# Optimization experiments

Measured on AMD Instinct MI355X. Metric: run time of the kernel, lower is better.

## Reference

```python
import jax, jax.numpy as jnp
import numpy as np

B, T, NR = 64, 128, 2
L, H, D = 8, 8, 512
HD = D // H
TMAX = T + 1  # block_size: U buffer has t+1 entries
U0 = jnp.array([191.713, 215.888], dtype=jnp.float32)


def _ln(x, w, b):
    mu = x.mean(-1, keepdims=True)
    var = ((x - mu) ** 2).mean(-1, keepdims=True)
    return (x - mu) * jax.lax.rsqrt(var + 1e-5) * w + b


def setup_inputs() -> dict:
    key = jax.random.key(0)
    ks = jax.random.split(key, 24)
    s = 0.02
    inp = {
        'data': jax.random.uniform(ks[0], (B, 4), jnp.float32),
        'r': jax.random.normal(ks[1], (B, T, NR), jnp.float32),
        'y_d': jax.random.normal(ks[2], (B, T, NR), jnp.float32),
        # token encoder: concat(e, u) -> D
        'wte_w': s * jax.random.normal(ks[3], (2 * NR, D), jnp.float32),
        'wte_b': jnp.zeros((D,), jnp.float32),
        'wpe': s * jax.random.normal(ks[4], (TMAX, D), jnp.float32),
        'ln1_w': jnp.ones((L, D), jnp.float32),
        'ln1_b': jnp.zeros((L, D), jnp.float32),
        'qkv_w': s * jax.random.normal(ks[5], (L, D, 3 * D), jnp.float32),
        'qkv_b': jnp.zeros((L, 3 * D), jnp.float32),
        'proj_w': s * jax.random.normal(ks[6], (L, D, D), jnp.float32),
        'proj_b': jnp.zeros((L, D), jnp.float32),
        'ln2_w': jnp.ones((L, D), jnp.float32),
        'ln2_b': jnp.zeros((L, D), jnp.float32),
        'fc_w': s * jax.random.normal(ks[7], (L, D, 4 * D), jnp.float32),
        'fc_b': jnp.zeros((L, 4 * D), jnp.float32),
        'mproj_w': s * jax.random.normal(ks[8], (L, 4 * D, D), jnp.float32),
        'mproj_b': jnp.zeros((L, D), jnp.float32),
        'lnf_w': jnp.ones((D,), jnp.float32),
        'lnf_b': jnp.zeros((D,), jnp.float32),
        'head_w': s * jax.random.normal(ks[9], (D, NR), jnp.float32),
        'head_b': jnp.zeros((NR,), jnp.float32),
    }
    return inp


def reference(data, r, y_d, wte_w, wte_b, wpe, ln1_w, ln1_b, qkv_w, qkv_b,
              proj_w, proj_b, ln2_w, ln2_b, fc_w, fc_b, mproj_w, mproj_b,
              lnf_w, lnf_b, head_w, head_b):
    # Incremental GPT decode with KV cache; math identical to recomputing
    # causal attention over the growing [E, U] prefix at every step.
    def gpt_step(token, pos, K, V):
        h = token @ wte_w + wte_b + wpe[pos]  # [B, D]
        for l in range(L):
            hn = _ln(h, ln1_w[l], ln1_b[l])
            qkv = hn @ qkv_w[l] + qkv_b[l]
            q, k, v = jnp.split(qkv, 3, axis=-1)
            q = q.reshape(B, H, HD)
            K = K.at[l, :, :, pos].set(k.reshape(B, H, HD))
            V = V.at[l, :, :, pos].set(v.reshape(B, H, HD))
            sc = jnp.einsum('bhd,bhtd->bht', q, K[l]) / jnp.sqrt(jnp.float32(HD))
            valid = jnp.arange(TMAX) <= pos
            sc = jnp.where(valid[None, None, :], sc, -jnp.inf)
            att = jax.nn.softmax(sc, axis=-1)
            o = jnp.einsum('bht,bhtd->bhd', att, V[l]).reshape(B, D)
            h = h + o @ proj_w[l] + proj_b[l]
            hn2 = _ln(h, ln2_w[l], ln2_b[l])
            h = h + jax.nn.gelu(hn2 @ fc_w[l] + fc_b[l], approximate=False) @ mproj_w[l] + mproj_b[l]
        h = _ln(h, lnf_w, lnf_b)
        return h @ head_w + head_b, K, V

    a_par = data[:, :NR]        # tmp params -> dynamics: x_dot = -a*x + b*u
    b_par = data[:, NR:2 * NR]

    def step(carry, r_i):
        y, u, K, V, i = carry
        e = r_i - y                       # e_i = r_i - y_i
        tok = jnp.concatenate([e, u], axis=-1)
        u_next, K, V = gpt_step(tok, i, K, V)
        x_dot = -a_par * y + b_par * u_next  # Ts = 1 Euler step
        y_next = y + x_dot
        return (y_next, u_next, K, V, i + 1), y

    K0 = jnp.zeros((L, B, H, TMAX, HD), jnp.float32)
    V0 = jnp.zeros((L, B, H, TMAX, HD), jnp.float32)
    u0 = jnp.broadcast_to(U0, (B, NR))
    y0 = y_d[:, 0, :]
    _, Y = jax.lax.scan(step, (y0, u0, K0, V0, jnp.int32(0)), jnp.swapaxes(r, 0, 1))
    return jnp.swapaxes(Y, 0, 1)  # [B, T, NR]
```

## Files before the change

kernel.cpp:

```cpp
#include <hip/hip_runtime.h>
#include <hip/hip_bf16.h>
#include <math.h>
#include <stdio.h>

#define NWG 256
#define NT  512
#define T_  128
#define L_  8
typedef unsigned short ushort_t;

struct P {
  const float *data,*r,*y_d,*wte_w,*wte_b,*wpe,*ln1_w,*ln1_b,*qkv_w,*qkv_b,
              *proj_w,*proj_b,*ln2_w,*ln2_b,*fc_w,*fc_b,*mproj_w,*mproj_b,
              *lnf_w,*lnf_b,*head_w,*head_b;
  float *out, *y, *u, *h0, *h1;
  ushort_t *qT, *oT, *gT;
  ushort_t *wq, *wp, *wf, *wm;
  ushort_t *Kc, *Vc;
  unsigned long long *sync;
};

__device__ __forceinline__ float bf2f(ushort_t u) {
  return __uint_as_float(((unsigned)u) << 16);
}
__device__ __forceinline__ ushort_t f2bf(float f) {
  __hip_bfloat16 b = __float2bfloat16(f);
  return *reinterpret_cast<ushort_t*>(&b);
}

__global__ void wconv(const float* __restrict__ src, ushort_t* __restrict__ dst, int n) {
  int i = blockIdx.x * blockDim.x + threadIdx.x;
  const int stride = gridDim.x * blockDim.x;
  for (; i < n; i += stride) dst[i] = f2bf(src[i]);
}

__device__ __forceinline__ void gbar(unsigned long long* gs, int xcd) {
  __syncthreads();
  if (threadIdx.x == 0) {
    unsigned long long* leaf = gs + xcd * 16;
    unsigned long long* root = gs + 128;
    unsigned long long* gen  = gs + 144;
    const unsigned long long g0 = __hip_atomic_load(gen, __ATOMIC_RELAXED, __HIP_MEMORY_SCOPE_AGENT);
    const unsigned long long lo = __hip_atomic_fetch_add(leaf, 1ULL, __ATOMIC_RELAXED, __HIP_MEMORY_SCOPE_AGENT);
    if (lo == 31ULL) {
      __hip_atomic_store(leaf, 0ULL, __ATOMIC_RELAXED, __HIP_MEMORY_SCOPE_AGENT);
      const unsigned long long ro = __hip_atomic_fetch_add(root, 1ULL, __ATOMIC_RELEASE, __HIP_MEMORY_SCOPE_AGENT);
      if (ro == 7ULL) {
        __hip_atomic_store(root, 0ULL, __ATOMIC_RELAXED, __HIP_MEMORY_SCOPE_AGENT);
        __hip_atomic_fetch_add(gen, 1ULL, __ATOMIC_RELEASE, __HIP_MEMORY_SCOPE_AGENT);
      }
    }
    while (__hip_atomic_load(gen, __ATOMIC_RELAXED, __HIP_MEMORY_SCOPE_AGENT) == g0)
      __builtin_amdgcn_s_sleep(2);
    (void)__hip_atomic_load(gen, __ATOMIC_ACQUIRE, __HIP_MEMORY_SCOPE_AGENT);
  }
  __syncthreads();
}

__device__ __forceinline__ int swz4(int k) { return ((k >> 1) & 3); }

__device__ __forceinline__ void stage_bf(const ushort_t* __restrict__ src, int W,
                                         int row0, int k0, float* slab) {
  const int tid = threadIdx.x;
  const int m = tid >> 5, q = tid & 31;
  const ushort_t* sp = src + (size_t)(row0 + m) * W + k0;
  #pragma unroll
  for (int i = 0; i < 16; ++i) {
    const int k = q + i * 32;
    slab[k * 16 + (m ^ (swz4(k) << 2))] = bf2f(sp[k]);
  }
}

__device__ __forceinline__ void stats_ln(const float* __restrict__ h,
                                         const float* __restrict__ lnw,
                                         const float* __restrict__ lnb,
                                         int rb, float* slab) {
  const int tid = threadIdx.x;
  const int m = tid >> 5, q = tid & 31;
  const float* hp = h + (size_t)(rb * 16 + m) * 512;
  float vv[16];
  float s = 0.f, s2 = 0.f;
  #pragma unroll
  for (int i = 0; i < 16; ++i) {
    const int k = q + i * 32;
    const float v = hp[k];
    vv[i] = v; s += v; s2 += v * v;
  }
  #pragma unroll
  for (int mk = 1; mk <= 16; mk <<= 1) { s += __shfl_xor(s, mk); s2 += __shfl_xor(s2, mk); }
  const float mu = s * (1.f / 512.f);
  const float rs = rsqrtf(s2 * (1.f / 512.f) - mu * mu + 1e-5f);
  #pragma unroll
  for (int i = 0; i < 16; ++i) {
    const int k = q + i * 32;
    slab[k * 16 + (m ^ (swz4(k) << 2))] = (vv[i] - mu) * rs * lnw[k] + lnb[k];
  }
}

#define FMA_ALL(W_, A_) \
  A_[0]+=W_*a0.x; A_[1]+=W_*a0.y; A_[2]+=W_*a0.z; A_[3]+=W_*a0.w; \
  A_[4]+=W_*a1.x; A_[5]+=W_*a1.y; A_[6]+=W_*a1.z; A_[7]+=W_*a1.w; \
  A_[8]+=W_*a2.x; A_[9]+=W_*a2.y; A_[10]+=W_*a2.z; A_[11]+=W_*a2.w; \
  A_[12]+=W_*a3.x; A_[13]+=W_*a3.y; A_[14]+=W_*a3.z; A_[15]+=W_*a3.w;

template<int N>
__device__ __forceinline__ void gemm_acc(const ushort_t* __restrict__ Wbase,
                                         const float* __restrict__ slab,
                                         float* acc0, float* acc1) {
  const int tid = threadIdx.x;
  const int wv = tid >> 6, lane = tid & 63;
  const int kq = lane >> 4, cp = lane & 15;
  const int r0 = wv * 64 + kq;
  const ushort_t* Wg = Wbase + (size_t)r0 * N + cp * 2;
  unsigned w[16];
  #pragma unroll
  for (int u = 0; u < 16; ++u)
    w[u] = *(const unsigned*)(Wg + (size_t)(u * 4) * N);
  #pragma unroll
  for (int u = 0; u < 16; ++u) {
    const int row = r0 + u * 4;
    const float4* b4 = (const float4*)(slab + row * 16);
    const int c4 = swz4(row);
    const float4 a0 = b4[0 ^ c4], a1 = b4[1 ^ c4], a2 = b4[2 ^ c4], a3 = b4[3 ^ c4];
    const float wx = bf2f((ushort_t)w[u]), wy = bf2f((ushort_t)(w[u] >> 16));
    FMA_ALL(wx, acc0)
    FMA_ALL(wy, acc1)
  }
}

__device__ __forceinline__ float gemm_finish(float* acc0, float* acc1, float* redw) {
  const int tid = threadIdx.x;
  const int wv = tid >> 6, lane = tid & 63;
  #pragma unroll
  for (int m = 0; m < 16; ++m) {
    acc0[m] += __shfl_xor(acc0[m], 16); acc1[m] += __shfl_xor(acc1[m], 16);
    acc0[m] += __shfl_xor(acc0[m], 32); acc1[m] += __shfl_xor(acc1[m], 32);
  }
  if (lane < 16) {
    float* rp = redw + wv * 528 + lane * 33;
    #pragma unroll
    for (int m = 0; m < 16; ++m) { rp[m] = acc0[m]; rp[16 + m] = acc1[m]; }
  }
  __syncthreads();
  const int col = tid & 31, m2 = tid >> 5;
  float s = 0.f;
  #pragma unroll
  for (int w2 = 0; w2 < 8; ++w2)
    s += redw[w2 * 528 + (col >> 1) * 33 + (col & 1) * 16 + m2];
  return s;
}

#define ACC_INIT float acc0[16], acc1[16]; \
  _Pragma("unroll") for (int m_ = 0; m_ < 16; ++m_) { acc0[m_] = 0.f; acc1[m_] = 0.f; }

__global__ __launch_bounds__(NT, 1) void gptloop(P p) {
  const int bid = blockIdx.x, tid = threadIdx.x;
  const int xcd = bid & 7, slot = bid >> 3;
  unsigned long long* sb = p.sync;

  __shared__ float slab[8192];
  __shared__ float redw[8 * 528];
  __shared__ float red1[512], red2[512];
  __shared__ float att_s[2][128];
  __shared__ float qv_s[2][64];
  __shared__ float inv_s[2];
  __shared__ float bc[4];

  if (slot < 8) {
    const int b = xcd * 8 + slot, t = tid;
    const float y0 = p.y_d[b * 256], y1 = p.y_d[b * 256 + 1];
    const float e0 = p.r[b * 256] - y0, e1 = p.r[b * 256 + 1] - y1;
    p.h0[b * 512 + t] = e0 * p.wte_w[t] + e1 * p.wte_w[512 + t]
                      + 191.713f * p.wte_w[1024 + t] + 215.888f * p.wte_w[1536 + t]
                      + p.wte_b[t] + p.wpe[t];
    if (t < 2) {
      p.y[b * 2 + t] = t ? y1 : y0;
      p.u[b * 2 + t] = t ? 215.888f : 191.713f;
    }
  }
  gbar(sb, xcd);

  for (int st = 0; st < T_; ++st) {
    for (int l = 0; l < L_; ++l) {
      if (slot < 24) {
        const int cb = xcd * 6 + (slot >> 2), rb = slot & 3;
        stats_ln(p.h0, p.ln1_w + l * 512, p.ln1_b + l * 512, rb, slab);
        __syncthreads();
        ACC_INIT
        gemm_acc<1536>(p.wq + (size_t)l * 786432 + cb * 32, slab, acc0, acc1);
        float v = gemm_finish(acc0, acc1, redw);
        const int col = tid & 31, m = tid >> 5;
        const int gcol = cb * 32 + col;
        v += p.qkv_b[l * 1536 + gcol];
        const int part = gcol >> 9, head = (gcol & 511) >> 6, off = gcol & 63;
        const int b = rb * 16 + m;
        if (part == 0) {
          p.qT[b * 512 + gcol] = f2bf(v * 0.125f);
        } else {
          ushort_t* dst = (part == 1) ? p.Kc : p.Vc;
          dst[((size_t)(l * 64 + b) * 8 + head) * 8192 + st * 64 + off] = f2bf(v);
        }
      }
      gbar(sb, xcd);

      {
        const int pp = tid >> 8, t = tid & 255;
        const int pid = bid * 2 + pp, b = pid >> 3, hh = pid & 7;
        const size_t kvb = ((size_t)(l * 64 + b) * 8 + hh) * (size_t)8192;
        if (t < 64) qv_s[pp][t] = bf2f(p.qT[b * 512 + hh * 64 + t]);
        __syncthreads();
        float s = -1e30f;
        if (t <= st && t < 128) {
          const uint4* kp = (const uint4*)(p.Kc + kvb + (size_t)t * 64);
          float sc = 0.f;
          #pragma unroll
          for (int j2 = 0; j2 < 8; ++j2) {
            const uint4 k4 = kp[j2];
            sc += qv_s[pp][j2*8+0] * bf2f((ushort_t)k4.x)
                + qv_s[pp][j2*8+1] * bf2f((ushort_t)(k4.x >> 16))
                + qv_s[pp][j2*8+2] * bf2f((ushort_t)k4.y)
                + qv_s[pp][j2*8+3] * bf2f((ushort_t)(k4.y >> 16))
                + qv_s[pp][j2*8+4] * bf2f((ushort_t)k4.z)
                + qv_s[pp][j2*8+5] * bf2f((ushort_t)(k4.z >> 16))
                + qv_s[pp][j2*8+6] * bf2f((ushort_t)k4.w)
                + qv_s[pp][j2*8+7] * bf2f((ushort_t)(k4.w >> 16));
          }
          s = sc;
        }
        red1[tid] = s; __syncthreads();
        for (int s2 = 128; s2 >= 1; s2 >>= 1) {
          if (t < s2) red1[tid] = fmaxf(red1[tid], red1[tid + s2]);
          __syncthreads();
        }
        const float mx = red1[pp * 256];
        __syncthreads();
        const float e = (t <= st && t < 128) ? expf(s - mx) : 0.f;
        if (t < 128) att_s[pp][t] = e;
        red1[tid] = e; __syncthreads();
        for (int s2 = 128; s2 >= 1; s2 >>= 1) {
          if (t < s2) red1[tid] += red1[tid + s2];
          __syncthreads();
        }
        if (t == 0) inv_s[pp] = 1.f / red1[pp * 256];
        __syncthreads();
        const int d = t & 63, tq = t >> 6;
        float o = 0.f;
        for (int tt = tq; tt <= st; tt += 4)
          o += att_s[pp][tt] * bf2f(p.Vc[kvb + (size_t)tt * 64 + d]);
        red1[tid] = o; __syncthreads();
        if (tid < 128) {
          const int p2 = tid >> 6, d2 = tid & 63;
          const int pid2 = bid * 2 + p2, b2 = pid2 >> 3, h2 = pid2 & 7;
          const float oo = (red1[p2*256 + d2] + red1[p2*256 + 64 + d2]
                          + red1[p2*256 + 128 + d2] + red1[p2*256 + 192 + d2]) * inv_s[p2];
          p.oT[b2 * 512 + h2 * 64 + d2] = f2bf(oo);
        }
      }
      gbar(sb, xcd);

      if (slot < 8) {
        const int cb = xcd * 2 + (slot >> 2), rb = slot & 3;
        stage_bf(p.oT, 512, rb * 16, 0, slab);
        __syncthreads();
        ACC_INIT
        gemm_acc<512>(p.wp + (size_t)l * 262144 + cb * 32, slab, acc0, acc1);
        const float v = gemm_finish(acc0, acc1, redw);
        const int col = tid & 31, m = tid >> 5;
        const int gcol = cb * 32 + col, row = rb * 16 + m;
        p.h1[row * 512 + gcol] = p.h0[row * 512 + gcol] + v + p.proj_b[l * 512 + gcol];
      }
      gbar(sb, xcd);

      {
        const int cb = xcd * 8 + (slot >> 2), rb = slot & 3;
        stats_ln(p.h1, p.ln2_w + l * 512, p.ln2_b + l * 512, rb, slab);
        __syncthreads();
        ACC_INIT
        gemm_acc<2048>(p.wf + (size_t)l * 1048576 + cb * 32, slab, acc0, acc1);
        const float v = gemm_finish(acc0, acc1, redw);
        const int col = tid & 31, m = tid >> 5;
        const int gcol = cb * 32 + col;
        const float x = v + p.fc_b[l * 2048 + gcol];
        p.gT[(size_t)(rb * 16 + m) * 2048 + gcol] =
            f2bf(0.5f * x * (1.f + erff(x * 0.70710678118654752f)));
      }
      gbar(sb, xcd);

      if (slot < 8) {
        const int cb = xcd * 2 + (slot >> 2), rb = slot & 3;
        ACC_INIT
        for (int ch = 0; ch < 4; ++ch) {
          __syncthreads();
          stage_bf(p.gT, 2048, rb * 16, ch * 512, slab);
          __syncthreads();
          gemm_acc<512>(p.wm + (size_t)l * 1048576 + (size_t)(ch * 512) * 512 + cb * 32,
                        slab, acc0, acc1);
        }
        const float v = gemm_finish(acc0, acc1, redw);
        const int col = tid & 31, m = tid >> 5;
        const int gcol = cb * 32 + col, row = rb * 16 + m;
        p.h0[row * 512 + gcol] = p.h1[row * 512 + gcol] + v + p.mproj_b[l * 512 + gcol];
      }
      gbar(sb, xcd);
    }

    if (slot < 8) {
      const int b = xcd * 8 + slot, t = tid;
      const float v = p.h0[b * 512 + t];
      red1[t] = v; red2[t] = v * v;
      __syncthreads();
      for (int s2 = 256; s2 >= 1; s2 >>= 1) {
        if (t < s2) { red1[t] += red1[t + s2]; red2[t] += red2[t + s2]; }
        __syncthreads();
      }
      const float mu = red1[0] * (1.f / 512.f);
      const float rs = rsqrtf(red2[0] * (1.f / 512.f) - mu * mu + 1e-5f);
      __syncthreads();
      const float hf = (v - mu) * rs * p.lnf_w[t] + p.lnf_b[t];
      red1[t] = hf * p.head_w[t * 2];
      red2[t] = hf * p.head_w[t * 2 + 1];
      __syncthreads();
      for (int s2 = 256; s2 >= 1; s2 >>= 1) {
        if (t < s2) { red1[t] += red1[t + s2]; red2[t] += red2[t + s2]; }
        __syncthreads();
      }
      if (t < 2) {
        const float un = ((t == 0) ? red1[0] : red2[0]) + p.head_b[t];
        const float a  = p.data[b * 4 + t];
        const float bb = p.data[b * 4 + 2 + t];
        const float yv = p.y[b * 2 + t];
        p.out[b * 256 + st * 2 + t] = yv;
        const float yn = yv - a * yv + bb * un;
        p.y[b * 2 + t] = yn;
        p.u[b * 2 + t] = un;
        bc[t] = yn; bc[2 + t] = un;
      }
      __syncthreads();
      if (st < T_ - 1) {
        const float e0 = p.r[b * 256 + (st + 1) * 2]     - bc[0];
        const float e1 = p.r[b * 256 + (st + 1) * 2 + 1] - bc[1];
        p.h0[b * 512 + t] = e0 * p.wte_w[t] + e1 * p.wte_w[512 + t]
                          + bc[2] * p.wte_w[1024 + t] + bc[3] * p.wte_w[1536 + t]
                          + p.wte_b[t] + p.wpe[(st + 1) * 512 + t];
      }
    }
    gbar(sb, xcd);
  }
}

extern "C" void kernel_launch(void* const* d_in, const int* in_sizes, int n_in,
                              void* d_out, int out_size, void* d_ws, size_t ws_size,
                              hipStream_t stream) {
  P p;
  p.data  =(const float*)d_in[0];  p.r      =(const float*)d_in[1];
  p.y_d   =(const float*)d_in[2];  p.wte_w  =(const float*)d_in[3];
  p.wte_b =(const float*)d_in[4];  p.wpe    =(const float*)d_in[5];
  p.ln1_w =(const float*)d_in[6];  p.ln1_b  =(const float*)d_in[7];
  p.qkv_w =(const float*)d_in[8];  p.qkv_b  =(const float*)d_in[9];
  p.proj_w=(const float*)d_in[10]; p.proj_b =(const float*)d_in[11];
  p.ln2_w =(const float*)d_in[12]; p.ln2_b =(const float*)d_in[13];
  p.fc_w  =(const float*)d_in[14]; p.fc_b   =(const float*)d_in[15];
  p.mproj_w=(const float*)d_in[16];p.mproj_b=(const float*)d_in[17];
  p.lnf_w =(const float*)d_in[18]; p.lnf_b  =(const float*)d_in[19];
  p.head_w=(const float*)d_in[20]; p.head_b =(const float*)d_in[21];
  p.out = (float*)d_out;

  char* w = (char*)d_ws;
  size_t off = 0;
  p.sync=(unsigned long long*)(w+off); off += 8192;
  p.y   =(float*)(w+off);          off += 512;
  p.u   =(float*)(w+off);          off += 512;
  p.h0  =(float*)(w+off);          off += (size_t)64*512*4;
  p.h1  =(float*)(w+off);          off += (size_t)64*512*4;
  p.qT  =(ushort_t*)(w+off);       off += (size_t)64*512*2;
  p.oT  =(ushort_t*)(w+off);       off += (size_t)64*512*2;
  p.gT  =(ushort_t*)(w+off);       off += (size_t)64*2048*2;
  p.wq  =(ushort_t*)(w+off);       off += (size_t)8*512*1536*2;
  p.wp  =(ushort_t*)(w+off);       off += (size_t)8*512*512*2;
  p.wf  =(ushort_t*)(w+off);       off += (size_t)8*512*2048*2;
  p.wm  =(ushort_t*)(w+off);       off += (size_t)8*2048*512*2;
  p.Kc  =(ushort_t*)(w+off);       off += (size_t)L_*64*8*T_*64*2;
  p.Vc  =(ushort_t*)(w+off);       off += (size_t)L_*64*8*T_*64*2;

  fprintf(stderr, "[gptloop] ws_size=%zu need=%zu\n", ws_size, off);
  if (ws_size < off) return;

  hipMemsetAsync(d_ws, 0, 8192, stream);
  hipLaunchKernelGGL(wconv, dim3(1024), dim3(256), 0, stream, p.qkv_w,  p.wq, 8*512*1536);
  hipLaunchKernelGGL(wconv, dim3(1024), dim3(256), 0, stream, p.proj_w, p.wp, 8*512*512);
  hipLaunchKernelGGL(wconv, dim3(1024), dim3(256), 0, stream, p.fc_w,   p.wf, 8*512*2048);
  hipLaunchKernelGGL(wconv, dim3(1024), dim3(256), 0, stream, p.mproj_w,p.wm, 8*2048*512);
  hipLaunchKernelGGL(gptloop, dim3(NWG), dim3(NT), 0, stream, p);
}
```

Measured before the change: 66.99 ms.

## Partition batch into four independent XCD-pair groups with local barriers

Splits the 256 workgroups into four groups, one per pair of XCDs, each owning 16 batch rows. Every group runs the whole layer pipeline for its own rows, so the grid-wide barrier becomes a 64-workgroup barrier per group with a smaller tree. The intent is to cut barrier latency and cross-XCD traffic, since batches are independent. In exchange, each group streams the full weight matrices for only 16 rows, which raises total weight reads and lowers GEMM reuse per row.

```diff
diff --git a/kernel.cpp b/kernel.cpp
--- a/kernel.cpp
+++ b/kernel.cpp
@@ -8,6 +8,7 @@
 #define T_  128
 #define L_  8
 typedef unsigned short ushort_t;
+typedef unsigned long long u64;
 
 struct P {
   const float *data,*r,*y_d,*wte_w,*wte_b,*wpe,*ln1_w,*ln1_b,*qkv_w,*qkv_b,
@@ -17,7 +18,7 @@
   ushort_t *qT, *oT, *gT;
   ushort_t *wq, *wp, *wf, *wm;
   ushort_t *Kc, *Vc;
-  unsigned long long *sync;
+  u64 *sync;
 };
 
 __device__ __forceinline__ float bf2f(ushort_t u) {
@@ -34,18 +35,18 @@
   for (; i < n; i += stride) dst[i] = f2bf(src[i]);
 }
 
-__device__ __forceinline__ void gbar(unsigned long long* gs, int xcd) {
+__device__ __forceinline__ void gbar(u64* gs, int lf) {
   __syncthreads();
   if (threadIdx.x == 0) {
-    unsigned long long* leaf = gs + xcd * 16;
-    unsigned long long* root = gs + 128;
-    unsigned long long* gen  = gs + 144;
-    const unsigned long long g0 = __hip_atomic_load(gen, __ATOMIC_RELAXED, __HIP_MEMORY_SCOPE_AGENT);
-    const unsigned long long lo = __hip_atomic_fetch_add(leaf, 1ULL, __ATOMIC_RELAXED, __HIP_MEMORY_SCOPE_AGENT);
+    u64* leaf = gs + lf * 16;
+    u64* root = gs + 32;
+    u64* gen  = gs + 48;
+    const u64 g0 = __hip_atomic_load(gen, __ATOMIC_RELAXED, __HIP_MEMORY_SCOPE_AGENT);
+    const u64 lo = __hip_atomic_fetch_add(leaf, 1ULL, __ATOMIC_RELAXED, __HIP_MEMORY_SCOPE_AGENT);
     if (lo == 31ULL) {
       __hip_atomic_store(leaf, 0ULL, __ATOMIC_RELAXED, __HIP_MEMORY_SCOPE_AGENT);
-      const unsigned long long ro = __hip_atomic_fetch_add(root, 1ULL, __ATOMIC_RELEASE, __HIP_MEMORY_SCOPE_AGENT);
-      if (ro == 7ULL) {
+      const u64 ro = __hip_atomic_fetch_add(root, 1ULL, __ATOMIC_RELEASE, __HIP_MEMORY_SCOPE_AGENT);
+      if (ro == 1ULL) {
         __hip_atomic_store(root, 0ULL, __ATOMIC_RELAXED, __HIP_MEMORY_SCOPE_AGENT);
         __hip_atomic_fetch_add(gen, 1ULL, __ATOMIC_RELEASE, __HIP_MEMORY_SCOPE_AGENT);
       }
@@ -155,8 +156,11 @@
 
 __global__ __launch_bounds__(NT, 1) void gptloop(P p) {
   const int bid = blockIdx.x, tid = threadIdx.x;
-  const int xcd = bid & 7, slot = bid >> 3;
-  unsigned long long* sb = p.sync;
+  const int xcd = bid & 7;
+  const int pr  = xcd >> 1;
+  const int lf  = bid & 1;
+  const int gw  = ((bid >> 3) << 1) | lf;
+  u64* gs = p.sync + pr * 512;
 
   __shared__ float slab[8192];
   __shared__ float redw[8 * 528];
@@ -166,8 +170,8 @@
   __shared__ float inv_s[2];
   __shared__ float bc[4];
 
-  if (slot < 8) {
-    const int b = xcd * 8 + slot, t = tid;
+  if (gw < 16) {
+    const int b = pr * 16 + gw, t = tid;
     const float y0 = p.y_d[b * 256], y1 = p.y_d[b * 256 + 1];
     const float e0 = p.r[b * 256] - y0, e1 = p.r[b * 256 + 1] - y1;
     p.h0[b * 512 + t] = e0 * p.wte_w[t] + e1 * p.wte_w[512 + t]
@@ -178,13 +182,13 @@
       p.u[b * 2 + t] = t ? 215.888f : 191.713f;
     }
   }
-  gbar(sb, xcd);
+  gbar(gs, lf);
 
   for (int st = 0; st < T_; ++st) {
     for (int l = 0; l < L_; ++l) {
-      if (slot < 24) {
-        const int cb = xcd * 6 + (slot >> 2), rb = slot & 3;
-        stats_ln(p.h0, p.ln1_w + l * 512, p.ln1_b + l * 512, rb, slab);
+      if (gw < 48) {
+        const int cb = gw;
+        stats_ln(p.h0, p.ln1_w + l * 512, p.ln1_b + l * 512, pr, slab);
         __syncthreads();
         ACC_INIT
         gemm_acc<1536>(p.wq + (size_t)l * 786432 + cb * 32, slab, acc0, acc1);
@@ -193,7 +197,7 @@
         const int gcol = cb * 32 + col;
         v += p.qkv_b[l * 1536 + gcol];
         const int part = gcol >> 9, head = (gcol & 511) >> 6, off = gcol & 63;
-        const int b = rb * 16 + m;
+        const int b = pr * 16 + m;
         if (part == 0) {
           p.qT[b * 512 + gcol] = f2bf(v * 0.125f);
         } else {
@@ -201,11 +205,12 @@
           dst[((size_t)(l * 64 + b) * 8 + head) * 8192 + st * 64 + off] = f2bf(v);
         }
       }
-      gbar(sb, xcd);
+      gbar(gs, lf);
 
       {
         const int pp = tid >> 8, t = tid & 255;
-        const int pid = bid * 2 + pp, b = pid >> 3, hh = pid & 7;
+        const int pidl = gw * 2 + pp;
+        const int b = pr * 16 + (pidl >> 3), hh = pidl & 7;
         const size_t kvb = ((size_t)(l * 64 + b) * 8 + hh) * (size_t)8192;
         if (t < 64) qv_s[pp][t] = bf2f(p.qT[b * 512 + hh * 64 + t]);
         __syncthreads();
@@ -250,30 +255,31 @@
         red1[tid] = o; __syncthreads();
         if (tid < 128) {
           const int p2 = tid >> 6, d2 = tid & 63;
-          const int pid2 = bid * 2 + p2, b2 = pid2 >> 3, h2 = pid2 & 7;
+          const int pidl2 = gw * 2 + p2;
+          const int b2 = pr * 16 + (pidl2 >> 3), h2 = pidl2 & 7;
           const float oo = (red1[p2*256 + d2] + red1[p2*256 + 64 + d2]
                           + red1[p2*256 + 128 + d2] + red1[p2*256 + 192 + d2]) * inv_s[p2];
           p.oT[b2 * 512 + h2 * 64 + d2] = f2bf(oo);
         }
       }
-      gbar(sb, xcd);
-
-      if (slot < 8) {
-        const int cb = xcd * 2 + (slot >> 2), rb = slot & 3;
-        stage_bf(p.oT, 512, rb * 16, 0, slab);
+      gbar(gs, lf);
+
+      if (gw < 16) {
+        const int cb = gw;
+        stage_bf(p.oT, 512, pr * 16, 0, slab);
         __syncthreads();
         ACC_INIT
         gemm_acc<512>(p.wp + (size_t)l * 262144 + cb * 32, slab, acc0, acc1);
         const float v = gemm_finish(acc0, acc1, redw);
         const int col = tid & 31, m = tid >> 5;
-        const int gcol = cb * 32 + col, row = rb * 16 + m;
+        const int gcol = cb * 32 + col, row = pr * 16 + m;
         p.h1[row * 512 + gcol] = p.h0[row * 512 + gcol] + v + p.proj_b[l * 512 + gcol];
       }
-      gbar(sb, xcd);
+      gbar(gs, lf);
 
       {
-        const int cb = xcd * 8 + (slot >> 2), rb = slot & 3;
-        stats_ln(p.h1, p.ln2_w + l * 512, p.ln2_b + l * 512, rb, slab);
+        const int cb = gw;
+        stats_ln(p.h1, p.ln2_w + l * 512, p.ln2_b + l * 512, pr, slab);
         __syncthreads();
         ACC_INIT
         gemm_acc<2048>(p.wf + (size_t)l * 1048576 + cb * 32, slab, acc0, acc1);
@@ -281,31 +287,31 @@
         const int col = tid & 31, m = tid >> 5;
         const int gcol = cb * 32 + col;
         const float x = v + p.fc_b[l * 2048 + gcol];
-        p.gT[(size_t)(rb * 16 + m) * 2048 + gcol] =
+        p.gT[(size_t)(pr * 16 + m) * 2048 + gcol] =
             f2bf(0.5f * x * (1.f + erff(x * 0.70710678118654752f)));
       }
-      gbar(sb, xcd);
-
-      if (slot < 8) {
-        const int cb = xcd * 2 + (slot >> 2), rb = slot & 3;
+      gbar(gs, lf);
+
+      if (gw < 16) {
+        const int cb = gw;
         ACC_INIT
         for (int ch = 0; ch < 4; ++ch) {
           __syncthreads();
-          stage_bf(p.gT, 2048, rb * 16, ch * 512, slab);
+          stage_bf(p.gT, 2048, pr * 16, ch * 512, slab);
           __syncthreads();
           gemm_acc<512>(p.wm + (size_t)l * 1048576 + (size_t)(ch * 512) * 512 + cb * 32,
                         slab, acc0, acc1);
         }
         const float v = gemm_finish(acc0, acc1, redw);
         const int col = tid & 31, m = tid >> 5;
-        const int gcol = cb * 32 + col, row = rb * 16 + m;
+        const int gcol = cb * 32 + col, row = pr * 16 + m;
         p.h0[row * 512 + gcol] = p.h1[row * 512 + gcol] + v + p.mproj_b[l * 512 + gcol];
       }
-      gbar(sb, xcd);
+      gbar(gs, lf);
     }
 
-    if (slot < 8) {
-      const int b = xcd * 8 + slot, t = tid;
+    if (gw < 16) {
+      const int b = pr * 16 + gw, t = tid;
       const float v = p.h0[b * 512 + t];
       red1[t] = v; red2[t] = v * v;
       __syncthreads();
@@ -344,7 +350,7 @@
                           + p.wte_b[t] + p.wpe[(st + 1) * 512 + t];
       }
     }
-    gbar(sb, xcd);
+    gbar(gs, lf);
   }
 }
 
@@ -358,7 +364,7 @@
   p.ln1_w =(const float*)d_in[6];  p.ln1_b  =(const float*)d_in[7];
   p.qkv_w =(const float*)d_in[8];  p.qkv_b  =(const float*)d_in[9];
   p.proj_w=(const float*)d_in[10]; p.proj_b =(const float*)d_in[11];
-  p.ln2_w =(const float*)d_in[12]; p.ln2_b =(const float*)d_in[13];
+  p.ln2_w =(const float*)d_in[12]; p.ln2_b  =(const float*)d_in[13];
   p.fc_w  =(const float*)d_in[14]; p.fc_b   =(const float*)d_in[15];
   p.mproj_w=(const float*)d_in[16];p.mproj_b=(const float*)d_in[17];
   p.lnf_w =(const float*)d_in[18]; p.lnf_b  =(const float*)d_in[19];
@@ -367,7 +373,7 @@
 
   char* w = (char*)d_ws;
   size_t off = 0;
-  p.sync=(unsigned long long*)(w+off); off += 8192;
+  p.sync=(u64*)(w+off);            off += 16384;
   p.y   =(float*)(w+off);          off += 512;
   p.u   =(float*)(w+off);          off += 512;
   p.h0  =(float*)(w+off);          off += (size_t)64*512*4;
@@ -385,7 +391,7 @@
   fprintf(stderr, "[gptloop] ws_size=%zu need=%zu\n", ws_size, off);
   if (ws_size < off) return;
 
-  hipMemsetAsync(d_ws, 0, 8192, stream);
+  hipMemsetAsync(d_ws, 0, 16384, stream);
   hipLaunchKernelGGL(wconv, dim3(1024), dim3(256), 0, stream, p.qkv_w,  p.wq, 8*512*1536);
   hipLaunchKernelGGL(wconv, dim3(1024), dim3(256), 0, stream, p.proj_w, p.wp, 8*512*512);
   hipLaunchKernelGGL(wconv, dim3(1024), dim3(256), 0, stream, p.fc_w,   p.wf, 8*512*2048);
```

New measurement: 68.19 ms. No clear change (+1.8%).
